# Kernel tuning notes

Hardware: AMD Instinct MI355X
Metric: run time of the kernel (lower is better)

Reference implementation:

```python
import jax, jax.numpy as jnp
import numpy as np
import math

H_IMG, W_IMG = 800, 1216
STRIDES = [4, 8, 16, 32, 64]
SIZES = [32, 64, 128, 256, 512]
RATIOS = [0.5, 1.0, 2.0]
NUM_PER_LEVEL = [(-(-H_IMG // s)) * (-(-W_IMG // s)) * len(RATIOS) for s in STRIDES]
A_TOTAL = sum(NUM_PER_LEVEL)  # 728973
B = 4
PRE_NMS = 1000   # pre_nms_top_n['testing']
POST_NMS = 1000  # post_nms_top_n['testing']
NMS_TH = 0.7
MIN_SIZE = 1e-3
BBOX_XFORM_CLIP = math.log(1000.0 / 16)
NEG = -1e10
LEVELS_NP = np.repeat(np.arange(len(NUM_PER_LEVEL)), NUM_PER_LEVEL).astype(np.int32)


def _make_anchors():
    out = []
    for stride, size in zip(STRIDES, SIZES):
        fh, fw = -(-H_IMG // stride), -(-W_IMG // stride)
        r = np.sqrt(np.asarray(RATIOS, dtype=np.float64))
        ws, hs = size / r, size * r
        base = np.stack([-ws / 2, -hs / 2, ws / 2, hs / 2], axis=1)  # [3,4]
        sx = np.arange(fw, dtype=np.float64) * stride
        sy = np.arange(fh, dtype=np.float64) * stride
        gy, gx = np.meshgrid(sy, sx, indexing='ij')
        shifts = np.stack([gx.ravel(), gy.ravel(), gx.ravel(), gy.ravel()], axis=1)
        out.append((shifts[:, None, :] + base[None]).reshape(-1, 4))
    return np.concatenate(out, 0).astype(np.float32)


def setup_inputs() -> dict:
    key = jax.random.key(0)
    k1, k2 = jax.random.split(key)
    objectness = jax.random.normal(k1, (B, A_TOTAL), dtype=jnp.float32)
    deltas = jax.random.normal(k2, (B, A_TOTAL, 4), dtype=jnp.float32) * 0.2
    anchors = jnp.asarray(_make_anchors())
    return {'objectness': objectness, 'deltas': deltas, 'anchors': anchors}


def _decode(deltas, anchors):
    # BoxCoder.decode with weights (1,1,1,1)
    wa = anchors[:, 2] - anchors[:, 0]
    ha = anchors[:, 3] - anchors[:, 1]
    cxa = anchors[:, 0] + 0.5 * wa
    cya = anchors[:, 1] + 0.5 * ha
    dx, dy = deltas[..., 0], deltas[..., 1]
    dw = jnp.minimum(deltas[..., 2], BBOX_XFORM_CLIP)
    dh = jnp.minimum(deltas[..., 3], BBOX_XFORM_CLIP)
    cx = dx * wa + cxa
    cy = dy * ha + cya
    w = jnp.exp(dw) * wa
    h = jnp.exp(dh) * ha
    return jnp.stack([cx - 0.5 * w, cy - 0.5 * h, cx + 0.5 * w, cy + 0.5 * h], axis=-1)


def _topk_per_level(obj):
    # _get_top_n_idx: independent top-k within each anchor level, indices offset
    idxs, off = [], 0
    for n in NUM_PER_LEVEL:
        k = min(PRE_NMS, n)
        _, ti = jax.lax.top_k(obj[:, off:off + n], k)
        idxs.append(ti + off)
        off += n
    return jnp.concatenate(idxs, axis=1)


def _pairwise_iou(b):
    area = (b[:, 2] - b[:, 0]) * (b[:, 3] - b[:, 1])
    lt = jnp.maximum(b[:, None, :2], b[None, :, :2])
    rb = jnp.minimum(b[:, None, 2:], b[None, :, 2:])
    wh = jnp.clip(rb - lt, 0.0)
    inter = wh[..., 0] * wh[..., 1]
    return inter / (area[:, None] + area[None, :] - inter)


def _filter_image(boxes, scores, lvl):
    # clip_boxes_to_image
    x1 = jnp.clip(boxes[:, 0], 0.0, W_IMG)
    y1 = jnp.clip(boxes[:, 1], 0.0, H_IMG)
    x2 = jnp.clip(boxes[:, 2], 0.0, W_IMG)
    y2 = jnp.clip(boxes[:, 3], 0.0, H_IMG)
    boxes = jnp.stack([x1, y1, x2, y2], axis=1)
    # remove_small_boxes (as a validity mask; fixed shapes under jit)
    valid = ((x2 - x1) >= MIN_SIZE) & ((y2 - y1) >= MIN_SIZE)
    scores = jnp.where(valid, scores, NEG)
    N = boxes.shape[0]
    # batched_nms: offset boxes per level so levels never overlap
    sg_boxes = jax.lax.stop_gradient(boxes)
    offset = lvl.astype(boxes.dtype) * (sg_boxes.max() + 1.0)
    order = jnp.argsort(-jax.lax.stop_gradient(scores))
    iou = _pairwise_iou(sg_boxes[order] + offset[order][:, None])  # [N,N]
    idx = jnp.arange(N)
    def body(i, keep):
        sup = (iou[i] > NMS_TH) & keep[i] & (idx > i)
        return keep & ~sup
    keep = jax.lax.fori_loop(0, N, body, valid[order])
    # kept entries in score order, then truncate to POST_NMS (fixed shape)
    prio = jnp.where(keep, idx, N)
    sel = jnp.argsort(prio)[:POST_NMS]
    kept = keep[sel]
    src = order[sel]
    out_b = jnp.where(kept[:, None], boxes[src], 0.0)
    out_s = jnp.where(kept, scores[src], NEG)
    return out_b, out_s


def reference(objectness, deltas, anchors):
    proposals = _decode(deltas, anchors)                      # [B,A,4]
    top_idx = _topk_per_level(objectness)                     # [B,5000]
    obj_sel = jnp.take_along_axis(objectness, top_idx, axis=1)
    prop_sel = jnp.take_along_axis(proposals, top_idx[..., None], axis=1)
    lvl_sel = jnp.asarray(LEVELS_NP)[top_idx]
    boxes, scores = jax.vmap(_filter_image)(prop_sel, obj_sel, lvl_sel)
    return boxes, scores  # [B,POST_NMS,4], [B,POST_NMS]
```

## Files before the change

### kernel.cpp

```cpp
#include <hip/hip_runtime.h>
#include <stdint.h>

#pragma clang fp contract(off)

#define B_IMGS   4
#define NLVL     5
#define A_TOTAL  242991
#define NSEL     4741
#define NBUCK    8192
#define BSHIFT   19
#define CAND_CAP 2048
#define POST_NMS 1000
#define NBL      (B_IMGS * NLVL)
#define NMS_TH   0.7f
#define NEGV     (-1e10f)
#define W_IMGF   1216.0f
#define H_IMGF   800.0f
#define MIN_SZ   1e-3f
#define BBOX_CLIP 4.135166556742356f

__device__ __forceinline__ int lvl_k(int l) { return (l == 4) ? 741 : 1000; }

__device__ __forceinline__ unsigned flipf(float f) {
    unsigned u = __float_as_uint(f);
    return u ^ (unsigned)(((int)u >> 31) | 0x80000000);
}
__device__ __forceinline__ float unflipf(unsigned os) {
    unsigned u = (os & 0x80000000u) ? (os ^ 0x80000000u) : ~os;
    return __uint_as_float(u);
}

__device__ __forceinline__ void async_cp16(const void* g, void* l) {
    __builtin_amdgcn_global_load_lds(
        (const __attribute__((address_space(1))) unsigned*)g,
        (__attribute__((address_space(3))) unsigned*)l,
        16, 0, 0);
}

static constexpr size_t SZ_HIST    = (size_t)NBL * NBUCK * sizeof(unsigned);
static constexpr size_t OFF_CNT    = SZ_HIST;
static constexpr size_t OFF_BOXMAX = OFF_CNT + NBL * sizeof(unsigned);
static constexpr size_t ZERO_BYTES = OFF_BOXMAX + B_IMGS * sizeof(unsigned);
static constexpr size_t OFF_CAND   = (ZERO_BYTES + 15) & ~(size_t)15;
static constexpr size_t OFF_SEL    = OFF_CAND + (size_t)NBL * CAND_CAP * 8;
static constexpr size_t OFF_BOXR   = OFF_SEL + (size_t)B_IMGS * NSEL * 8;
static constexpr size_t OFF_SCR    = OFF_BOXR + (size_t)B_IMGS * NSEL * 16;
static constexpr size_t OFF_BOXL   = OFF_SCR + (size_t)B_IMGS * NSEL * 4;
static constexpr size_t OFF_VAL    = OFF_BOXL + (size_t)B_IMGS * NSEL * 16;
static constexpr size_t OFF_RMAP   = OFF_VAL + (size_t)B_IMGS * NSEL * 4;
static constexpr size_t OFF_KEEP   = OFF_RMAP + (size_t)B_IMGS * NSEL * 4;
static constexpr size_t OFF_MASK   = OFF_KEEP + (size_t)B_IMGS * NSEL * 4;
static constexpr size_t WS_NEED    = OFF_MASK + (size_t)NBL * 1024 * 16 * 8;

#define HBLK_PER_IMG 34
__global__ void k_hist(const float* __restrict__ obj, unsigned* __restrict__ hist) {
    __shared__ unsigned lh[NBUCK];
    const int tid = threadIdx.x;
    const int b = blockIdx.x / HBLK_PER_IMG;
    const int r = blockIdx.x - b * HBLK_PER_IMG;
    int l, sub, chunk, lstart, n;
    if (r < 24)      { l = 0; sub = r;      chunk = 7600; lstart = 0;      n = 182400; }
    else if (r < 30) { l = 1; sub = r - 24; chunk = 7600; lstart = 182400; n = 45600; }
    else if (r < 32) { l = 2; sub = r - 30; chunk = 5700; lstart = 228000; n = 11400; }
    else if (r == 32){ l = 3; sub = 0;      chunk = 2850; lstart = 239400; n = 2850; }
    else             { l = 4; sub = 0;      chunk = 741;  lstart = 242250; n = 741; }
    #pragma unroll
    for (int i = tid; i < NBUCK; i += 512) lh[i] = 0;
    __syncthreads();
    const int s0 = sub * chunk;
    const int cnt = min(chunk, n - s0);
    const float* src = obj + (size_t)b * A_TOTAL + lstart + s0;
    for (int i = tid; i < cnt; i += 512) {
        unsigned os = flipf(src[i]);
        atomicAdd(&lh[os >> BSHIFT], 1u);
    }
    __syncthreads();
    unsigned* gh = hist + (size_t)(b * NLVL + l) * NBUCK;
    for (int i = tid; i < NBUCK; i += 512) {
        unsigned v = lh[i];
        if (v) atomicAdd(&gh[i], v);
    }
}

#define CBLK_PER_IMG 65
__global__ void k_compact(const float* __restrict__ obj, const unsigned* __restrict__ hist,
                          unsigned* __restrict__ cnt, unsigned long long* __restrict__ cand) {
    __shared__ unsigned long long sbuf[CAND_CAP];
    __shared__ unsigned part[256];
    __shared__ unsigned chunkbuf[32];
    __shared__ int s_chunk;
    __shared__ unsigned s_cum, s_thr, lcnt, gbase;
    const int tid = threadIdx.x;
    const int b = blockIdx.x / CBLK_PER_IMG;
    const int r = blockIdx.x - b * CBLK_PER_IMG;
    int l, sub, chunk, lstart, n;
    if (r < 48)      { l = 0; sub = r;      chunk = 3800; lstart = 0;      n = 182400; }
    else if (r < 60) { l = 1; sub = r - 48; chunk = 3800; lstart = 182400; n = 45600; }
    else if (r < 63) { l = 2; sub = r - 60; chunk = 3800; lstart = 228000; n = 11400; }
    else if (r == 63){ l = 3; sub = 0;      chunk = 2850; lstart = 239400; n = 2850; }
    else             { l = 4; sub = 0;      chunk = 741;  lstart = 242250; n = 741; }
    const int bl = b * NLVL + l;
    const int kl = lvl_k(l);
    const unsigned* h = hist + (size_t)bl * NBUCK;
    {
        unsigned s = 0;
        for (int i = 0; i < 32; ++i) s += h[tid * 32 + i];
        part[tid] = s;
    }
    if (tid == 0) lcnt = 0;
    __syncthreads();
    if (tid == 0) {
        unsigned cum = 0;
        int t = 255;
        for (; t > 0; --t) {
            if (cum + part[t] >= (unsigned)kl) break;
            cum += part[t];
        }
        s_chunk = t;
        s_cum = cum;
    }
    __syncthreads();
    if (tid < 32) chunkbuf[tid] = h[s_chunk * 32 + tid];
    __syncthreads();
    if (tid == 0) {
        unsigned c2 = s_cum;
        int T = s_chunk * 32;
        for (int i = 31; i >= 0; --i) {
            c2 += chunkbuf[i];
            if (c2 >= (unsigned)kl) { T = s_chunk * 32 + i; break; }
        }
        s_thr = (unsigned)T;
    }
    __syncthreads();
    const unsigned T = s_thr;
    const int s0 = sub * chunk;
    const int m = min(chunk, n - s0);
    const int abase = lstart + s0;
    const float* src = obj + (size_t)b * A_TOTAL + abase;
    for (int i = tid; i < m; i += 256) {
        unsigned os = flipf(src[i]);
        if ((os >> BSHIFT) >= T) {
            unsigned slot = atomicAdd(&lcnt, 1u);
            if (slot < CAND_CAP)
                sbuf[slot] = (((unsigned long long)(~os)) << 32) | (unsigned)(abase + i);
        }
    }
    __syncthreads();
    unsigned total = lcnt; if (total > CAND_CAP) total = CAND_CAP;
    if (tid == 0) gbase = atomicAdd(&cnt[bl], total);
    __syncthreads();
    const unsigned gb = gbase;
    for (unsigned i = tid; i < total; i += 256) {
        unsigned g = gb + i;
        if (g < CAND_CAP)
            cand[(size_t)bl * CAND_CAP + g] = sbuf[i];
    }
}

__global__ void k_sortlevel(const unsigned long long* __restrict__ cand,
                            const unsigned* __restrict__ cnt,
                            unsigned long long* __restrict__ sel) {
    __shared__ unsigned long long keys[CAND_CAP];
    const int bl = blockIdx.x;
    const int b = bl / NLVL, l = bl - (bl / NLVL) * NLVL;
    const int tid = threadIdx.x;
    int m = (int)cnt[bl];
    if (m > CAND_CAP) m = CAND_CAP;
    for (int i = tid; i < CAND_CAP; i += 512)
        keys[i] = (i < m) ? cand[(size_t)bl * CAND_CAP + i] : ~0ULL;
    __syncthreads();
    for (int k = 2; k <= CAND_CAP; k <<= 1) {
        for (int j = k >> 1; j > 0; j >>= 1) {
            for (int t = tid; t < CAND_CAP / 2; t += 512) {
                int i = ((t / j) * (j << 1)) + (t % j);
                int p = i + j;
                bool up = ((i & k) == 0);
                unsigned long long a = keys[i], c = keys[p];
                if ((a > c) == up) { keys[i] = c; keys[p] = a; }
            }
            __syncthreads();
        }
    }
    int kl = lvl_k(l);
    for (int q = tid; q < kl; q += 512)
        sel[(size_t)b * NSEL + l * 1000 + q] = keys[q];
}

__device__ __forceinline__ int lbound_lds(const unsigned long long* s, int len,
                                          unsigned long long key) {
    int lo = 0, hi = len;
    while (lo < hi) {
        int mid = (lo + hi) >> 1;
        if (s[mid] < key) lo = mid + 1; else hi = mid;
    }
    return lo;
}

__global__ void k_decode(const float* __restrict__ deltas, const float* __restrict__ anchors,
                         const unsigned long long* __restrict__ sel,
                         float* __restrict__ boxes_r, float* __restrict__ score_r,
                         float* __restrict__ boxes_l, int* __restrict__ valid_l,
                         int* __restrict__ rankmap, unsigned* __restrict__ boxmax) {
    __shared__ unsigned long long skey[NSEL];
    __shared__ float wmax[16];
    const int b = blockIdx.y;
    const int tid = threadIdx.x;
    for (int i = tid; i < NSEL; i += 1024)
        skey[i] = sel[(size_t)b * NSEL + i];
    __syncthreads();

    int p = blockIdx.x * 1024 + tid;
    bool on = p < NSEL;
    float mx = 0.0f;
    if (on) {
        int l = p / 1000;
        int q = p - l * 1000;
        unsigned long long key = skey[p];
        unsigned a = (unsigned)(key & 0xFFFFFFFFu);
        unsigned os = ~((unsigned)(key >> 32));
        if (a >= A_TOTAL) a = 0;
        float score = unflipf(os);
        int r = q;
        for (int l2 = 0; l2 < NLVL; ++l2) {
            if (l2 == l) continue;
            r += lbound_lds(skey + l2 * 1000, lvl_k(l2), key);
        }
        const float* dv = deltas + ((size_t)b * A_TOTAL + a) * 4;
        const float* av = anchors + (size_t)a * 4;
        float ax1 = av[0], ay1 = av[1], ax2 = av[2], ay2 = av[3];
        float wa = ax2 - ax1, ha = ay2 - ay1;
        float cxa = ax1 + 0.5f * wa, cya = ay1 + 0.5f * ha;
        float dx = dv[0], dy = dv[1];
        float dw = fminf(dv[2], BBOX_CLIP), dh = fminf(dv[3], BBOX_CLIP);
        float cx = dx * wa + cxa, cy = dy * ha + cya;
        float w = expf(dw) * wa, h = expf(dh) * ha;
        float x1 = cx - 0.5f * w, y1 = cy - 0.5f * h;
        float x2 = cx + 0.5f * w, y2 = cy + 0.5f * h;
        float x1c = fminf(fmaxf(x1, 0.0f), W_IMGF);
        float y1c = fminf(fmaxf(y1, 0.0f), H_IMGF);
        float x2c = fminf(fmaxf(x2, 0.0f), W_IMGF);
        float y2c = fminf(fmaxf(y2, 0.0f), H_IMGF);
        int valid = ((x2c - x1c) >= MIN_SZ) && ((y2c - y1c) >= MIN_SZ);
        mx = fmaxf(fmaxf(x1c, y1c), fmaxf(x2c, y2c));
        size_t rp = (size_t)b * NSEL + r;
        boxes_r[rp * 4 + 0] = x1c; boxes_r[rp * 4 + 1] = y1c;
        boxes_r[rp * 4 + 2] = x2c; boxes_r[rp * 4 + 3] = y2c;
        score_r[rp] = score;
        size_t pp = (size_t)b * NSEL + p;
        boxes_l[pp * 4 + 0] = x1c; boxes_l[pp * 4 + 1] = y1c;
        boxes_l[pp * 4 + 2] = x2c; boxes_l[pp * 4 + 3] = y2c;
        valid_l[pp] = valid;
        rankmap[pp] = r;
    }
    #pragma unroll
    for (int o = 32; o > 0; o >>= 1)
        mx = fmaxf(mx, __shfl_xor(mx, o));
    if ((tid & 63) == 0) wmax[tid >> 6] = mx;
    __syncthreads();
    if (tid == 0) {
        float m2 = wmax[0];
        #pragma unroll
        for (int i = 1; i < 16; ++i) m2 = fmaxf(m2, wmax[i]);
        atomicMax(boxmax + b, __float_as_uint(m2));
    }
}

__global__ void k_mask(const float* __restrict__ boxes_l, const unsigned* __restrict__ boxmax,
                       unsigned long long* __restrict__ mask) {
    int bl = blockIdx.z;
    int b = bl / NLVL, l = bl - b * NLVL;
    int kl = lvl_k(l);
    int w = blockIdx.x, rg = blockIdx.y, tid = threadIdx.x;
    if (rg * 256 >= kl) return;
    float M = __uint_as_float(boxmax[b]) + 1.0f;
    float off = (float)l * M;
    __shared__ float cb[64][5];
    int j0 = w * 64;
    if (tid < 64) {
        int j = j0 + tid;
        if (j < kl) {
            const float* bp = boxes_l + ((size_t)b * NSEL + l * 1000 + j) * 4;
            float x1 = bp[0] + off, y1 = bp[1] + off, x2 = bp[2] + off, y2 = bp[3] + off;
            cb[tid][0] = x1; cb[tid][1] = y1; cb[tid][2] = x2; cb[tid][3] = y2;
            cb[tid][4] = (x2 - x1) * (y2 - y1);
        }
    }
    __syncthreads();
    int i = rg * 256 + tid;
    if (i >= kl) return;
    unsigned long long word = 0;
    if (j0 + 63 > i) {
        const float* bp = boxes_l + ((size_t)b * NSEL + l * 1000 + i) * 4;
        float ix1 = bp[0] + off, iy1 = bp[1] + off, ix2 = bp[2] + off, iy2 = bp[3] + off;
        float ai = (ix2 - ix1) * (iy2 - iy1);
        int jmax = min(64, kl - j0);
        for (int bb = 0; bb < jmax; ++bb) {
            int jj = j0 + bb;
            if (jj <= i) continue;
            float ltx = fmaxf(ix1, cb[bb][0]), lty = fmaxf(iy1, cb[bb][1]);
            float rbx = fminf(ix2, cb[bb][2]), rby = fminf(iy2, cb[bb][3]);
            float ww = fmaxf(rbx - ltx, 0.0f), hh = fmaxf(rby - lty, 0.0f);
            float inter = ww * hh;
            float iou = inter / ((ai + cb[bb][4]) - inter);
            if (iou > NMS_TH) word |= (1ULL << bb);
        }
    }
    mask[((size_t)bl * 1024 + i) * 16 + w] = word;
}

__global__ void k_resolve(const int* __restrict__ valid_l, const int* __restrict__ rankmap,
                          const unsigned long long* __restrict__ mask, int* __restrict__ keep_r) {
    const int bl = blockIdx.x;
    const int b = bl / NLVL, l = bl - b * NLVL;
    const int kl = lvl_k(l);
    const int lane = threadIdx.x;
    __shared__ __align__(16) unsigned long long sbufA[64 * 16];
    __shared__ __align__(16) unsigned long long sbufB[64 * 16];
    const int base = b * NSEL + l * 1000;

    unsigned long long keep_w = 0;
    for (int c = 0; c < 16; ++c) {
        int q = c * 64 + lane;
        int vv = (q < kl) ? valid_l[base + q] : 0;
        unsigned long long bm = __ballot(vv);
        if (lane == c) keep_w = bm;
    }

    const int nch = (kl + 63) >> 6;
    const char* mbyte = (const char*)(mask + (size_t)bl * 1024 * 16);

    {
        const char* g0 = mbyte + (size_t)lane * 16;
        #pragma unroll
        for (int j = 0; j < 8; ++j)
            async_cp16(g0 + j * 1024, (char*)sbufA + j * 1024);
    }

    for (int c = 0; c < nch; ++c) {
        unsigned long long* cur = (c & 1) ? sbufB : sbufA;
        unsigned long long* nxt = (c & 1) ? sbufA : sbufB;
        __syncthreads();
        if (c + 1 < nch) {
            const char* g1 = mbyte + (size_t)(c + 1) * 8192 + (size_t)lane * 16;
            #pragma unroll
            for (int j = 0; j < 8; ++j)
                async_cp16(g1 + j * 1024, (char*)nxt + j * 1024);
        }
        unsigned long long kw = __shfl(keep_w, c);
        if (kw) {
            unsigned long long diag = cur[lane * 16 + c];
            unsigned dlo = (unsigned)diag, dhi = (unsigned)(diag >> 32);
            unsigned long long nz = __ballot(diag != 0ULL);
            unsigned long long rem = kw & nz;
            while (rem) {
                int r = __ffsll((long long)rem) - 1;
                unsigned lo = __builtin_amdgcn_readlane(dlo, r);
                unsigned hi = __builtin_amdgcn_readlane(dhi, r);
                unsigned long long d = ((unsigned long long)hi << 32) | lo;
                kw &= ~d;
                rem &= ~(d | (1ULL << r));
            }
            unsigned long long supp = 0;
            if (lane < 16) {
                #pragma unroll
                for (int r = 0; r < 64; ++r) {
                    unsigned long long m = cur[r * 16 + lane];
                    supp |= (((kw >> r) & 1ULL) ? m : 0ULL);
                }
            }
            if (lane == c) keep_w = kw;
            else if (lane < 16 && lane > c) keep_w &= ~supp;
        }
    }
    __syncthreads();
    for (int c = 0; c < 16; ++c) {
        unsigned long long kwc = __shfl(keep_w, c);
        int q = c * 64 + lane;
        if (q < kl)
            keep_r[b * NSEL + rankmap[base + q]] = (int)((kwc >> lane) & 1ULL);
    }
}

__global__ void k_output(const int* __restrict__ keep_r, const float* __restrict__ boxes_r,
                         const float* __restrict__ score_r, float* __restrict__ out) {
    int b = blockIdx.x, tid = threadIdx.x;
    float* ob = out + (size_t)b * POST_NMS * 4;
    float* osc = out + (size_t)B_IMGS * POST_NMS * 4 + (size_t)b * POST_NMS;
    for (int p = tid; p < POST_NMS; p += 1024) {
        ob[p * 4 + 0] = 0.0f; ob[p * 4 + 1] = 0.0f;
        ob[p * 4 + 2] = 0.0f; ob[p * 4 + 3] = 0.0f;
        osc[p] = NEGV;
    }
    __syncthreads();
    const int CH = 5;
    int base = tid * CH;
    int cnt = 0;
    #pragma unroll
    for (int k = 0; k < CH; ++k) {
        int r = base + k;
        if (r < NSEL) cnt += keep_r[b * NSEL + r];
    }
    __shared__ int ps[1024];
    ps[tid] = cnt;
    __syncthreads();
    for (int ofs = 1; ofs < 1024; ofs <<= 1) {
        int v = (tid >= ofs) ? ps[tid - ofs] : 0;
        __syncthreads();
        ps[tid] += v;
        __syncthreads();
    }
    int p = ps[tid] - cnt;
    #pragma unroll
    for (int k = 0; k < CH; ++k) {
        int r = base + k;
        if (r < NSEL && keep_r[b * NSEL + r]) {
            if (p < POST_NMS) {
                const float* bp = boxes_r + ((size_t)b * NSEL + r) * 4;
                ob[p * 4 + 0] = bp[0]; ob[p * 4 + 1] = bp[1];
                ob[p * 4 + 2] = bp[2]; ob[p * 4 + 3] = bp[3];
                osc[p] = score_r[(size_t)b * NSEL + r];
            }
            ++p;
        }
    }
}

extern "C" void kernel_launch(void* const* d_in, const int* in_sizes, int n_in,
                              void* d_out, int out_size, void* d_ws, size_t ws_size,
                              hipStream_t stream) {
    const float* obj     = (const float*)d_in[0];
    const float* deltas  = (const float*)d_in[1];
    const float* anchors = (const float*)d_in[2];
    float* out = (float*)d_out;

    char* ws = (char*)d_ws;
    unsigned*            hist    = (unsigned*)(ws);
    unsigned*            cnt     = (unsigned*)(ws + OFF_CNT);
    unsigned*            boxmax  = (unsigned*)(ws + OFF_BOXMAX);
    unsigned long long*  cand    = (unsigned long long*)(ws + OFF_CAND);
    unsigned long long*  sel     = (unsigned long long*)(ws + OFF_SEL);
    float*               boxes_r = (float*)(ws + OFF_BOXR);
    float*               score_r = (float*)(ws + OFF_SCR);
    float*               boxes_l = (float*)(ws + OFF_BOXL);
    int*                 valid_l = (int*)(ws + OFF_VAL);
    int*                 rankmap = (int*)(ws + OFF_RMAP);
    int*                 keep_r  = (int*)(ws + OFF_KEEP);
    unsigned long long*  maskp   = (unsigned long long*)(ws + OFF_MASK);

    (void)in_sizes; (void)n_in; (void)out_size; (void)ws_size; (void)WS_NEED;

    hipMemsetAsync(d_ws, 0, ZERO_BYTES, stream);

    k_hist<<<B_IMGS * HBLK_PER_IMG, 512, 0, stream>>>(obj, hist);
    k_compact<<<B_IMGS * CBLK_PER_IMG, 256, 0, stream>>>(obj, hist, cnt, cand);
    k_sortlevel<<<NBL, 512, 0, stream>>>(cand, cnt, sel);
    k_decode<<<dim3(5, B_IMGS), 1024, 0, stream>>>(
        deltas, anchors, sel, boxes_r, score_r, boxes_l, valid_l, rankmap, boxmax);
    k_mask<<<dim3(16, 4, NBL), 256, 0, stream>>>(boxes_l, boxmax, maskp);
    k_resolve<<<NBL, 64, 0, stream>>>(valid_l, rankmap, maskp, keep_r);
    k_output<<<B_IMGS, 1024, 0, stream>>>(keep_r, boxes_r, score_r, out);
}
```

Baseline: 193.5 us.

## Fuse all RPN stages into one persistent kernel with grid barriers

Replaces seven separate kernel launches with a single persistent kernel of 136 blocks that runs histogram, compaction, per-level sort, decode, mask building, NMS resolve and output as phases separated by atomic-counter grid barriers. This removes per-launch overhead and the idle gaps between small dependent kernels. The price is less parallelism in some phases (compaction uses 136 blocks instead of 260, mask work is looped over blocks), fixed block sizes for every stage, and correctness that depends on all blocks being co-resident.

New measurement: 246.9 us. 1.28x slower.

```diff
diff --git a/kernel.cpp b/kernel.cpp
--- a/kernel.cpp
+++ b/kernel.cpp
@@ -19,7 +19,20 @@
 #define MIN_SZ   1e-3f
 #define BBOX_CLIP 4.135166556742356f
 
+#define NBLK     136
+#define BLKT     512
+#define HBLK_PER_IMG 34
+
 __device__ __forceinline__ int lvl_k(int l) { return (l == 4) ? 741 : 1000; }
+
+__device__ __forceinline__ void span34(int r, int& l, int& sub, int& chunk,
+                                       int& lstart, int& n) {
+    if (r < 24)      { l = 0; sub = r;      chunk = 7600; lstart = 0;      n = 182400; }
+    else if (r < 30) { l = 1; sub = r - 24; chunk = 7600; lstart = 182400; n = 45600; }
+    else if (r < 32) { l = 2; sub = r - 30; chunk = 5700; lstart = 228000; n = 11400; }
+    else if (r == 32){ l = 3; sub = 0;      chunk = 2850; lstart = 239400; n = 2850; }
+    else             { l = 4; sub = 0;      chunk = 741;  lstart = 242250; n = 741; }
+}
 
 __device__ __forceinline__ unsigned flipf(float f) {
     unsigned u = __float_as_uint(f);
@@ -37,10 +50,33 @@
         16, 0, 0);
 }
 
+__device__ __forceinline__ int lbound_lds(const unsigned long long* s, int len,
+                                          unsigned long long key) {
+    int lo = 0, hi = len;
+    while (lo < hi) {
+        int mid = (lo + hi) >> 1;
+        if (s[mid] < key) lo = mid + 1; else hi = mid;
+    }
+    return lo;
+}
+
+__device__ __forceinline__ void gbar(unsigned* bar, unsigned target) {
+    __syncthreads();
+    if (threadIdx.x == 0) {
+        __threadfence();
+        __hip_atomic_fetch_add(bar, 1u, __ATOMIC_RELAXED, __HIP_MEMORY_SCOPE_AGENT);
+        while (__hip_atomic_load(bar, __ATOMIC_RELAXED, __HIP_MEMORY_SCOPE_AGENT) < target)
+            __builtin_amdgcn_s_sleep(8);
+        __threadfence();
+    }
+    __syncthreads();
+}
+
 static constexpr size_t SZ_HIST    = (size_t)NBL * NBUCK * sizeof(unsigned);
 static constexpr size_t OFF_CNT    = SZ_HIST;
 static constexpr size_t OFF_BOXMAX = OFF_CNT + NBL * sizeof(unsigned);
-static constexpr size_t ZERO_BYTES = OFF_BOXMAX + B_IMGS * sizeof(unsigned);
+static constexpr size_t OFF_BAR    = OFF_BOXMAX + B_IMGS * sizeof(unsigned);
+static constexpr size_t ZERO_BYTES = OFF_BAR + 16;
 static constexpr size_t OFF_CAND   = (ZERO_BYTES + 15) & ~(size_t)15;
 static constexpr size_t OFF_SEL    = OFF_CAND + (size_t)NBL * CAND_CAP * 8;
 static constexpr size_t OFF_BOXR   = OFF_SEL + (size_t)B_IMGS * NSEL * 8;
@@ -52,375 +88,372 @@
 static constexpr size_t OFF_MASK   = OFF_KEEP + (size_t)B_IMGS * NSEL * 4;
 static constexpr size_t WS_NEED    = OFF_MASK + (size_t)NBL * 1024 * 16 * 8;
 
-#define HBLK_PER_IMG 34
-__global__ void k_hist(const float* __restrict__ obj, unsigned* __restrict__ hist) {
-    __shared__ unsigned lh[NBUCK];
+__global__ __launch_bounds__(BLKT, 2) void k_fused(
+    const float* __restrict__ obj, const float* __restrict__ deltas,
+    const float* __restrict__ anchors,
+    unsigned* __restrict__ hist, unsigned* __restrict__ cnt,
+    unsigned* __restrict__ boxmax, unsigned* __restrict__ bar,
+    unsigned long long* __restrict__ cand, unsigned long long* __restrict__ sel,
+    float* __restrict__ boxes_r, float* __restrict__ score_r,
+    float* __restrict__ boxes_l, int* __restrict__ valid_l,
+    int* __restrict__ rankmap, int* __restrict__ keep_r,
+    unsigned long long* __restrict__ maskp, float* __restrict__ out)
+{
+    __shared__ __align__(16) char smem[38912];
     const int tid = threadIdx.x;
-    const int b = blockIdx.x / HBLK_PER_IMG;
-    const int r = blockIdx.x - b * HBLK_PER_IMG;
-    int l, sub, chunk, lstart, n;
-    if (r < 24)      { l = 0; sub = r;      chunk = 7600; lstart = 0;      n = 182400; }
-    else if (r < 30) { l = 1; sub = r - 24; chunk = 7600; lstart = 182400; n = 45600; }
-    else if (r < 32) { l = 2; sub = r - 30; chunk = 5700; lstart = 228000; n = 11400; }
-    else if (r == 32){ l = 3; sub = 0;      chunk = 2850; lstart = 239400; n = 2850; }
-    else             { l = 4; sub = 0;      chunk = 741;  lstart = 242250; n = 741; }
-    #pragma unroll
-    for (int i = tid; i < NBUCK; i += 512) lh[i] = 0;
-    __syncthreads();
-    const int s0 = sub * chunk;
-    const int cnt = min(chunk, n - s0);
-    const float* src = obj + (size_t)b * A_TOTAL + lstart + s0;
-    for (int i = tid; i < cnt; i += 512) {
-        unsigned os = flipf(src[i]);
-        atomicAdd(&lh[os >> BSHIFT], 1u);
-    }
-    __syncthreads();
-    unsigned* gh = hist + (size_t)(b * NLVL + l) * NBUCK;
-    for (int i = tid; i < NBUCK; i += 512) {
-        unsigned v = lh[i];
-        if (v) atomicAdd(&gh[i], v);
-    }
-}
-
-#define CBLK_PER_IMG 65
-__global__ void k_compact(const float* __restrict__ obj, const unsigned* __restrict__ hist,
-                          unsigned* __restrict__ cnt, unsigned long long* __restrict__ cand) {
-    __shared__ unsigned long long sbuf[CAND_CAP];
-    __shared__ unsigned part[256];
-    __shared__ unsigned chunkbuf[32];
-    __shared__ int s_chunk;
-    __shared__ unsigned s_cum, s_thr, lcnt, gbase;
-    const int tid = threadIdx.x;
-    const int b = blockIdx.x / CBLK_PER_IMG;
-    const int r = blockIdx.x - b * CBLK_PER_IMG;
-    int l, sub, chunk, lstart, n;
-    if (r < 48)      { l = 0; sub = r;      chunk = 3800; lstart = 0;      n = 182400; }
-    else if (r < 60) { l = 1; sub = r - 48; chunk = 3800; lstart = 182400; n = 45600; }
-    else if (r < 63) { l = 2; sub = r - 60; chunk = 3800; lstart = 228000; n = 11400; }
-    else if (r == 63){ l = 3; sub = 0;      chunk = 2850; lstart = 239400; n = 2850; }
-    else             { l = 4; sub = 0;      chunk = 741;  lstart = 242250; n = 741; }
-    const int bl = b * NLVL + l;
-    const int kl = lvl_k(l);
-    const unsigned* h = hist + (size_t)bl * NBUCK;
+    const int bid = blockIdx.x;
+
     {
-        unsigned s = 0;
-        for (int i = 0; i < 32; ++i) s += h[tid * 32 + i];
-        part[tid] = s;
-    }
-    if (tid == 0) lcnt = 0;
-    __syncthreads();
-    if (tid == 0) {
-        unsigned cum = 0;
-        int t = 255;
-        for (; t > 0; --t) {
-            if (cum + part[t] >= (unsigned)kl) break;
-            cum += part[t];
-        }
-        s_chunk = t;
-        s_cum = cum;
-    }
-    __syncthreads();
-    if (tid < 32) chunkbuf[tid] = h[s_chunk * 32 + tid];
-    __syncthreads();
-    if (tid == 0) {
-        unsigned c2 = s_cum;
-        int T = s_chunk * 32;
-        for (int i = 31; i >= 0; --i) {
-            c2 += chunkbuf[i];
-            if (c2 >= (unsigned)kl) { T = s_chunk * 32 + i; break; }
-        }
-        s_thr = (unsigned)T;
-    }
-    __syncthreads();
-    const unsigned T = s_thr;
-    const int s0 = sub * chunk;
-    const int m = min(chunk, n - s0);
-    const int abase = lstart + s0;
-    const float* src = obj + (size_t)b * A_TOTAL + abase;
-    for (int i = tid; i < m; i += 256) {
-        unsigned os = flipf(src[i]);
-        if ((os >> BSHIFT) >= T) {
-            unsigned slot = atomicAdd(&lcnt, 1u);
-            if (slot < CAND_CAP)
-                sbuf[slot] = (((unsigned long long)(~os)) << 32) | (unsigned)(abase + i);
-        }
-    }
-    __syncthreads();
-    unsigned total = lcnt; if (total > CAND_CAP) total = CAND_CAP;
-    if (tid == 0) gbase = atomicAdd(&cnt[bl], total);
-    __syncthreads();
-    const unsigned gb = gbase;
-    for (unsigned i = tid; i < total; i += 256) {
-        unsigned g = gb + i;
-        if (g < CAND_CAP)
-            cand[(size_t)bl * CAND_CAP + g] = sbuf[i];
-    }
-}
-
-__global__ void k_sortlevel(const unsigned long long* __restrict__ cand,
-                            const unsigned* __restrict__ cnt,
-                            unsigned long long* __restrict__ sel) {
-    __shared__ unsigned long long keys[CAND_CAP];
-    const int bl = blockIdx.x;
-    const int b = bl / NLVL, l = bl - (bl / NLVL) * NLVL;
-    const int tid = threadIdx.x;
-    int m = (int)cnt[bl];
-    if (m > CAND_CAP) m = CAND_CAP;
-    for (int i = tid; i < CAND_CAP; i += 512)
-        keys[i] = (i < m) ? cand[(size_t)bl * CAND_CAP + i] : ~0ULL;
-    __syncthreads();
-    for (int k = 2; k <= CAND_CAP; k <<= 1) {
-        for (int j = k >> 1; j > 0; j >>= 1) {
-            for (int t = tid; t < CAND_CAP / 2; t += 512) {
-                int i = ((t / j) * (j << 1)) + (t % j);
-                int p = i + j;
-                bool up = ((i & k) == 0);
-                unsigned long long a = keys[i], c = keys[p];
-                if ((a > c) == up) { keys[i] = c; keys[p] = a; }
-            }
+        unsigned* lh = (unsigned*)smem;
+        const int b = bid / HBLK_PER_IMG;
+        const int r = bid - b * HBLK_PER_IMG;
+        int l, sub, chunk, lstart, n;
+        span34(r, l, sub, chunk, lstart, n);
+        for (int i = tid; i < NBUCK; i += BLKT) lh[i] = 0;
+        __syncthreads();
+        const int s0 = sub * chunk;
+        const int m = min(chunk, n - s0);
+        const float* src = obj + (size_t)b * A_TOTAL + lstart + s0;
+        for (int i = tid; i < m; i += BLKT) {
+            unsigned os = flipf(src[i]);
+            atomicAdd(&lh[os >> BSHIFT], 1u);
+        }
+        __syncthreads();
+        unsigned* gh = hist + (size_t)(b * NLVL + l) * NBUCK;
+        for (int i = tid; i < NBUCK; i += BLKT) {
+            unsigned v = lh[i];
+            if (v) atomicAdd(&gh[i], v);
+        }
+    }
+    gbar(bar, 1u * NBLK);
+
+    {
+        unsigned long long* sbuf = (unsigned long long*)smem;
+        unsigned* part     = (unsigned*)(smem + 16384);
+        unsigned* chunkbuf = (unsigned*)(smem + 17408);
+        int*      s_chunk  = (int*)     (smem + 17536);
+        unsigned* s_cum    = (unsigned*)(smem + 17540);
+        unsigned* s_thr    = (unsigned*)(smem + 17544);
+        unsigned* lcnt     = (unsigned*)(smem + 17548);
+        unsigned* gbase    = (unsigned*)(smem + 17552);
+        const int b = bid / HBLK_PER_IMG;
+        const int r = bid - b * HBLK_PER_IMG;
+        int l, sub, chunk, lstart, n;
+        span34(r, l, sub, chunk, lstart, n);
+        const int bl = b * NLVL + l;
+        const int kl = lvl_k(l);
+        const unsigned* h = hist + (size_t)bl * NBUCK;
+        if (tid < 256) {
+            unsigned s = 0;
+            for (int i = 0; i < 32; ++i) s += h[tid * 32 + i];
+            part[tid] = s;
+        }
+        if (tid == 0) *lcnt = 0;
+        __syncthreads();
+        if (tid == 0) {
+            unsigned cum = 0;
+            int t = 255;
+            for (; t > 0; --t) {
+                if (cum + part[t] >= (unsigned)kl) break;
+                cum += part[t];
+            }
+            *s_chunk = t;
+            *s_cum = cum;
+        }
+        __syncthreads();
+        if (tid < 32) chunkbuf[tid] = h[(*s_chunk) * 32 + tid];
+        __syncthreads();
+        if (tid == 0) {
+            unsigned c2 = *s_cum;
+            int T = (*s_chunk) * 32;
+            for (int i = 31; i >= 0; --i) {
+                c2 += chunkbuf[i];
+                if (c2 >= (unsigned)kl) { T = (*s_chunk) * 32 + i; break; }
+            }
+            *s_thr = (unsigned)T;
+        }
+        __syncthreads();
+        const unsigned T = *s_thr;
+        const int s0 = sub * chunk;
+        const int m = min(chunk, n - s0);
+        const int abase = lstart + s0;
+        const float* src = obj + (size_t)b * A_TOTAL + abase;
+        for (int i = tid; i < m; i += BLKT) {
+            unsigned os = flipf(src[i]);
+            if ((os >> BSHIFT) >= T) {
+                unsigned slot = atomicAdd(lcnt, 1u);
+                if (slot < CAND_CAP)
+                    sbuf[slot] = (((unsigned long long)(~os)) << 32) | (unsigned)(abase + i);
+            }
+        }
+        __syncthreads();
+        unsigned total = *lcnt; if (total > CAND_CAP) total = CAND_CAP;
+        if (tid == 0) *gbase = atomicAdd(&cnt[bl], total);
+        __syncthreads();
+        const unsigned gb = *gbase;
+        for (unsigned i = tid; i < total; i += BLKT) {
+            unsigned g = gb + i;
+            if (g < CAND_CAP)
+                cand[(size_t)bl * CAND_CAP + g] = sbuf[i];
+        }
+    }
+    gbar(bar, 2u * NBLK);
+
+    if (bid < NBL) {
+        unsigned long long* keys = (unsigned long long*)smem;
+        const int bl = bid;
+        const int b = bl / NLVL, l = bl - b * NLVL;
+        int m = (int)cnt[bl];
+        if (m > CAND_CAP) m = CAND_CAP;
+        for (int i = tid; i < CAND_CAP; i += BLKT)
+            keys[i] = (i < m) ? cand[(size_t)bl * CAND_CAP + i] : ~0ULL;
+        __syncthreads();
+        for (int k = 2; k <= CAND_CAP; k <<= 1) {
+            for (int j = k >> 1; j > 0; j >>= 1) {
+                for (int t = tid; t < CAND_CAP / 2; t += BLKT) {
+                    int i = ((t / j) * (j << 1)) + (t % j);
+                    int p = i + j;
+                    bool up = ((i & k) == 0);
+                    unsigned long long a = keys[i], c = keys[p];
+                    if ((a > c) == up) { keys[i] = c; keys[p] = a; }
+                }
+                __syncthreads();
+            }
+        }
+        int kl = lvl_k(l);
+        for (int q = tid; q < kl; q += BLKT)
+            sel[(size_t)b * NSEL + l * 1000 + q] = keys[q];
+    }
+    gbar(bar, 3u * NBLK);
+
+    if (bid < B_IMGS * 10) {
+        unsigned long long* skey = (unsigned long long*)smem;
+        float* wmax = (float*)(smem + 37928);
+        const int b = bid / 10;
+        const int sub = bid - b * 10;
+        for (int i = tid; i < NSEL; i += BLKT)
+            skey[i] = sel[(size_t)b * NSEL + i];
+        __syncthreads();
+
+        int p = sub * BLKT + tid;
+        bool on = p < NSEL;
+        float mx = 0.0f;
+        if (on) {
+            int l = p / 1000;
+            int q = p - l * 1000;
+            unsigned long long key = skey[p];
+            unsigned a = (unsigned)(key & 0xFFFFFFFFu);
+            unsigned os = ~((unsigned)(key >> 32));
+            if (a >= A_TOTAL) a = 0;
+            float score = unflipf(os);
+            int r = q;
+            for (int l2 = 0; l2 < NLVL; ++l2) {
+                if (l2 == l) continue;
+                r += lbound_lds(skey + l2 * 1000, lvl_k(l2), key);
+            }
+            const float* dv = deltas + ((size_t)b * A_TOTAL + a) * 4;
+            const float* av = anchors + (size_t)a * 4;
+            float ax1 = av[0], ay1 = av[1], ax2 = av[2], ay2 = av[3];
+            float wa = ax2 - ax1, ha = ay2 - ay1;
+            float cxa = ax1 + 0.5f * wa, cya = ay1 + 0.5f * ha;
+            float dx = dv[0], dy = dv[1];
+            float dw = fminf(dv[2], BBOX_CLIP), dh = fminf(dv[3], BBOX_CLIP);
+            float cx = dx * wa + cxa, cy = dy * ha + cya;
+            float w = expf(dw) * wa, h = expf(dh) * ha;
+            float x1 = cx - 0.5f * w, y1 = cy - 0.5f * h;
+            float x2 = cx + 0.5f * w, y2 = cy + 0.5f * h;
+            float x1c = fminf(fmaxf(x1, 0.0f), W_IMGF);
+            float y1c = fminf(fmaxf(y1, 0.0f), H_IMGF);
+            float x2c = fminf(fmaxf(x2, 0.0f), W_IMGF);
+            float y2c = fminf(fmaxf(y2, 0.0f), H_IMGF);
+            int valid = ((x2c - x1c) >= MIN_SZ) && ((y2c - y1c) >= MIN_SZ);
+            mx = fmaxf(fmaxf(x1c, y1c), fmaxf(x2c, y2c));
+            size_t rp = (size_t)b * NSEL + r;
+            boxes_r[rp * 4 + 0] = x1c; boxes_r[rp * 4 + 1] = y1c;
+            boxes_r[rp * 4 + 2] = x2c; boxes_r[rp * 4 + 3] = y2c;
+            score_r[rp] = score;
+            size_t pp = (size_t)b * NSEL + p;
+            boxes_l[pp * 4 + 0] = x1c; boxes_l[pp * 4 + 1] = y1c;
+            boxes_l[pp * 4 + 2] = x2c; boxes_l[pp * 4 + 3] = y2c;
+            valid_l[pp] = valid;
+            rankmap[pp] = r;
+        }
+        #pragma unroll
+        for (int o = 32; o > 0; o >>= 1)
+            mx = fmaxf(mx, __shfl_xor(mx, o));
+        if ((tid & 63) == 0) wmax[tid >> 6] = mx;
+        __syncthreads();
+        if (tid == 0) {
+            float m2 = wmax[0];
+            #pragma unroll
+            for (int i = 1; i < 8; ++i) m2 = fmaxf(m2, wmax[i]);
+            atomicMax(boxmax + b, __float_as_uint(m2));
+        }
+    }
+    gbar(bar, 4u * NBLK);
+
+    {
+        float (*cb)[5] = (float(*)[5])smem;
+        for (int u = bid; u < 640; u += NBLK) {
+            int w = u & 15, rg2 = (u >> 4) & 1, bl = u >> 5;
+            int b = bl / NLVL, l = bl - b * NLVL;
+            int kl = lvl_k(l);
+            bool act = (rg2 * BLKT < kl);
+            float M = __uint_as_float(boxmax[b]) + 1.0f;
+            float off = (float)l * M;
+            int j0 = w * 64;
             __syncthreads();
-        }
-    }
-    int kl = lvl_k(l);
-    for (int q = tid; q < kl; q += 512)
-        sel[(size_t)b * NSEL + l * 1000 + q] = keys[q];
-}
-
-__device__ __forceinline__ int lbound_lds(const unsigned long long* s, int len,
-                                          unsigned long long key) {
-    int lo = 0, hi = len;
-    while (lo < hi) {
-        int mid = (lo + hi) >> 1;
-        if (s[mid] < key) lo = mid + 1; else hi = mid;
-    }
-    return lo;
-}
-
-__global__ void k_decode(const float* __restrict__ deltas, const float* __restrict__ anchors,
-                         const unsigned long long* __restrict__ sel,
-                         float* __restrict__ boxes_r, float* __restrict__ score_r,
-                         float* __restrict__ boxes_l, int* __restrict__ valid_l,
-                         int* __restrict__ rankmap, unsigned* __restrict__ boxmax) {
-    __shared__ unsigned long long skey[NSEL];
-    __shared__ float wmax[16];
-    const int b = blockIdx.y;
-    const int tid = threadIdx.x;
-    for (int i = tid; i < NSEL; i += 1024)
-        skey[i] = sel[(size_t)b * NSEL + i];
-    __syncthreads();
-
-    int p = blockIdx.x * 1024 + tid;
-    bool on = p < NSEL;
-    float mx = 0.0f;
-    if (on) {
-        int l = p / 1000;
-        int q = p - l * 1000;
-        unsigned long long key = skey[p];
-        unsigned a = (unsigned)(key & 0xFFFFFFFFu);
-        unsigned os = ~((unsigned)(key >> 32));
-        if (a >= A_TOTAL) a = 0;
-        float score = unflipf(os);
-        int r = q;
-        for (int l2 = 0; l2 < NLVL; ++l2) {
-            if (l2 == l) continue;
-            r += lbound_lds(skey + l2 * 1000, lvl_k(l2), key);
-        }
-        const float* dv = deltas + ((size_t)b * A_TOTAL + a) * 4;
-        const float* av = anchors + (size_t)a * 4;
-        float ax1 = av[0], ay1 = av[1], ax2 = av[2], ay2 = av[3];
-        float wa = ax2 - ax1, ha = ay2 - ay1;
-        float cxa = ax1 + 0.5f * wa, cya = ay1 + 0.5f * ha;
-        float dx = dv[0], dy = dv[1];
-        float dw = fminf(dv[2], BBOX_CLIP), dh = fminf(dv[3], BBOX_CLIP);
-        float cx = dx * wa + cxa, cy = dy * ha + cya;
-        float w = expf(dw) * wa, h = expf(dh) * ha;
-        float x1 = cx - 0.5f * w, y1 = cy - 0.5f * h;
-        float x2 = cx + 0.5f * w, y2 = cy + 0.5f * h;
-        float x1c = fminf(fmaxf(x1, 0.0f), W_IMGF);
-        float y1c = fminf(fmaxf(y1, 0.0f), H_IMGF);
-        float x2c = fminf(fmaxf(x2, 0.0f), W_IMGF);
-        float y2c = fminf(fmaxf(y2, 0.0f), H_IMGF);
-        int valid = ((x2c - x1c) >= MIN_SZ) && ((y2c - y1c) >= MIN_SZ);
-        mx = fmaxf(fmaxf(x1c, y1c), fmaxf(x2c, y2c));
-        size_t rp = (size_t)b * NSEL + r;
-        boxes_r[rp * 4 + 0] = x1c; boxes_r[rp * 4 + 1] = y1c;
-        boxes_r[rp * 4 + 2] = x2c; boxes_r[rp * 4 + 3] = y2c;
-        score_r[rp] = score;
-        size_t pp = (size_t)b * NSEL + p;
-        boxes_l[pp * 4 + 0] = x1c; boxes_l[pp * 4 + 1] = y1c;
-        boxes_l[pp * 4 + 2] = x2c; boxes_l[pp * 4 + 3] = y2c;
-        valid_l[pp] = valid;
-        rankmap[pp] = r;
-    }
-    #pragma unroll
-    for (int o = 32; o > 0; o >>= 1)
-        mx = fmaxf(mx, __shfl_xor(mx, o));
-    if ((tid & 63) == 0) wmax[tid >> 6] = mx;
-    __syncthreads();
-    if (tid == 0) {
-        float m2 = wmax[0];
-        #pragma unroll
-        for (int i = 1; i < 16; ++i) m2 = fmaxf(m2, wmax[i]);
-        atomicMax(boxmax + b, __float_as_uint(m2));
-    }
-}
-
-__global__ void k_mask(const float* __restrict__ boxes_l, const unsigned* __restrict__ boxmax,
-                       unsigned long long* __restrict__ mask) {
-    int bl = blockIdx.z;
-    int b = bl / NLVL, l = bl - b * NLVL;
-    int kl = lvl_k(l);
-    int w = blockIdx.x, rg = blockIdx.y, tid = threadIdx.x;
-    if (rg * 256 >= kl) return;
-    float M = __uint_as_float(boxmax[b]) + 1.0f;
-    float off = (float)l * M;
-    __shared__ float cb[64][5];
-    int j0 = w * 64;
-    if (tid < 64) {
-        int j = j0 + tid;
-        if (j < kl) {
-            const float* bp = boxes_l + ((size_t)b * NSEL + l * 1000 + j) * 4;
-            float x1 = bp[0] + off, y1 = bp[1] + off, x2 = bp[2] + off, y2 = bp[3] + off;
-            cb[tid][0] = x1; cb[tid][1] = y1; cb[tid][2] = x2; cb[tid][3] = y2;
-            cb[tid][4] = (x2 - x1) * (y2 - y1);
-        }
-    }
-    __syncthreads();
-    int i = rg * 256 + tid;
-    if (i >= kl) return;
-    unsigned long long word = 0;
-    if (j0 + 63 > i) {
-        const float* bp = boxes_l + ((size_t)b * NSEL + l * 1000 + i) * 4;
-        float ix1 = bp[0] + off, iy1 = bp[1] + off, ix2 = bp[2] + off, iy2 = bp[3] + off;
-        float ai = (ix2 - ix1) * (iy2 - iy1);
-        int jmax = min(64, kl - j0);
-        for (int bb = 0; bb < jmax; ++bb) {
-            int jj = j0 + bb;
-            if (jj <= i) continue;
-            float ltx = fmaxf(ix1, cb[bb][0]), lty = fmaxf(iy1, cb[bb][1]);
-            float rbx = fminf(ix2, cb[bb][2]), rby = fminf(iy2, cb[bb][3]);
-            float ww = fmaxf(rbx - ltx, 0.0f), hh = fmaxf(rby - lty, 0.0f);
-            float inter = ww * hh;
-            float iou = inter / ((ai + cb[bb][4]) - inter);
-            if (iou > NMS_TH) word |= (1ULL << bb);
-        }
-    }
-    mask[((size_t)bl * 1024 + i) * 16 + w] = word;
-}
-
-__global__ void k_resolve(const int* __restrict__ valid_l, const int* __restrict__ rankmap,
-                          const unsigned long long* __restrict__ mask, int* __restrict__ keep_r) {
-    const int bl = blockIdx.x;
-    const int b = bl / NLVL, l = bl - b * NLVL;
-    const int kl = lvl_k(l);
-    const int lane = threadIdx.x;
-    __shared__ __align__(16) unsigned long long sbufA[64 * 16];
-    __shared__ __align__(16) unsigned long long sbufB[64 * 16];
-    const int base = b * NSEL + l * 1000;
-
-    unsigned long long keep_w = 0;
-    for (int c = 0; c < 16; ++c) {
-        int q = c * 64 + lane;
-        int vv = (q < kl) ? valid_l[base + q] : 0;
-        unsigned long long bm = __ballot(vv);
-        if (lane == c) keep_w = bm;
-    }
-
-    const int nch = (kl + 63) >> 6;
-    const char* mbyte = (const char*)(mask + (size_t)bl * 1024 * 16);
-
-    {
-        const char* g0 = mbyte + (size_t)lane * 16;
-        #pragma unroll
-        for (int j = 0; j < 8; ++j)
-            async_cp16(g0 + j * 1024, (char*)sbufA + j * 1024);
-    }
-
-    for (int c = 0; c < nch; ++c) {
-        unsigned long long* cur = (c & 1) ? sbufB : sbufA;
-        unsigned long long* nxt = (c & 1) ? sbufA : sbufB;
-        __syncthreads();
-        if (c + 1 < nch) {
-            const char* g1 = mbyte + (size_t)(c + 1) * 8192 + (size_t)lane * 16;
+            if (act && tid < 64) {
+                int j = j0 + tid;
+                if (j < kl) {
+                    const float* bp = boxes_l + ((size_t)b * NSEL + l * 1000 + j) * 4;
+                    float x1 = bp[0] + off, y1 = bp[1] + off;
+                    float x2 = bp[2] + off, y2 = bp[3] + off;
+                    cb[tid][0] = x1; cb[tid][1] = y1; cb[tid][2] = x2; cb[tid][3] = y2;
+                    cb[tid][4] = (x2 - x1) * (y2 - y1);
+                }
+            }
+            __syncthreads();
+            int i = rg2 * BLKT + tid;
+            if (act && i < kl) {
+                unsigned long long word = 0;
+                if (j0 + 63 > i) {
+                    const float* bp = boxes_l + ((size_t)b * NSEL + l * 1000 + i) * 4;
+                    float ix1 = bp[0] + off, iy1 = bp[1] + off;
+                    float ix2 = bp[2] + off, iy2 = bp[3] + off;
+                    float ai = (ix2 - ix1) * (iy2 - iy1);
+                    int jmax = min(64, kl - j0);
+                    for (int bb = 0; bb < jmax; ++bb) {
+                        int jj = j0 + bb;
+                        if (jj <= i) continue;
+                        float ltx = fmaxf(ix1, cb[bb][0]), lty = fmaxf(iy1, cb[bb][1]);
+                        float rbx = fminf(ix2, cb[bb][2]), rby = fminf(iy2, cb[bb][3]);
+                        float ww = fmaxf(rbx - ltx, 0.0f), hh = fmaxf(rby - lty, 0.0f);
+                        float inter = ww * hh;
+                        float iou = inter / ((ai + cb[bb][4]) - inter);
+                        if (iou > NMS_TH) word |= (1ULL << bb);
+                    }
+                }
+                maskp[((size_t)bl * 1024 + i) * 16 + w] = word;
+            }
+        }
+    }
+    gbar(bar, 5u * NBLK);
+
+    if (bid < NBL) {
+        const int bl = bid;
+        const int b = bl / NLVL, l = bl - b * NLVL;
+        const int kl = lvl_k(l);
+        const int lane = tid;
+        unsigned long long* sA = (unsigned long long*)smem;
+        unsigned long long* sB = (unsigned long long*)(smem + 8192);
+        const int base = b * NSEL + l * 1000;
+        unsigned long long keep_w = 0;
+        const int nch = (kl + 63) >> 6;
+        const char* mbyte = (const char*)(maskp + (size_t)bl * 1024 * 16);
+
+        if (tid < 64) {
+            for (int c = 0; c < 16; ++c) {
+                int q = c * 64 + lane;
+                int vv = (q < kl) ? valid_l[base + q] : 0;
+                unsigned long long bm = __ballot(vv);
+                if (lane == c) keep_w = bm;
+            }
+            const char* g0 = mbyte + (size_t)lane * 16;
             #pragma unroll
             for (int j = 0; j < 8; ++j)
-                async_cp16(g1 + j * 1024, (char*)nxt + j * 1024);
-        }
-        unsigned long long kw = __shfl(keep_w, c);
-        if (kw) {
-            unsigned long long diag = cur[lane * 16 + c];
-            unsigned dlo = (unsigned)diag, dhi = (unsigned)(diag >> 32);
-            unsigned long long nz = __ballot(diag != 0ULL);
-            unsigned long long rem = kw & nz;
-            while (rem) {
-                int r = __ffsll((long long)rem) - 1;
-                unsigned lo = __builtin_amdgcn_readlane(dlo, r);
-                unsigned hi = __builtin_amdgcn_readlane(dhi, r);
-                unsigned long long d = ((unsigned long long)hi << 32) | lo;
-                kw &= ~d;
-                rem &= ~(d | (1ULL << r));
-            }
-            unsigned long long supp = 0;
-            if (lane < 16) {
-                #pragma unroll
-                for (int r = 0; r < 64; ++r) {
-                    unsigned long long m = cur[r * 16 + lane];
-                    supp |= (((kw >> r) & 1ULL) ? m : 0ULL);
-                }
-            }
-            if (lane == c) keep_w = kw;
-            else if (lane < 16 && lane > c) keep_w &= ~supp;
-        }
-    }
-    __syncthreads();
-    for (int c = 0; c < 16; ++c) {
-        unsigned long long kwc = __shfl(keep_w, c);
-        int q = c * 64 + lane;
-        if (q < kl)
-            keep_r[b * NSEL + rankmap[base + q]] = (int)((kwc >> lane) & 1ULL);
-    }
-}
-
-__global__ void k_output(const int* __restrict__ keep_r, const float* __restrict__ boxes_r,
-                         const float* __restrict__ score_r, float* __restrict__ out) {
-    int b = blockIdx.x, tid = threadIdx.x;
-    float* ob = out + (size_t)b * POST_NMS * 4;
-    float* osc = out + (size_t)B_IMGS * POST_NMS * 4 + (size_t)b * POST_NMS;
-    for (int p = tid; p < POST_NMS; p += 1024) {
-        ob[p * 4 + 0] = 0.0f; ob[p * 4 + 1] = 0.0f;
-        ob[p * 4 + 2] = 0.0f; ob[p * 4 + 3] = 0.0f;
-        osc[p] = NEGV;
-    }
-    __syncthreads();
-    const int CH = 5;
-    int base = tid * CH;
-    int cnt = 0;
-    #pragma unroll
-    for (int k = 0; k < CH; ++k) {
-        int r = base + k;
-        if (r < NSEL) cnt += keep_r[b * NSEL + r];
-    }
-    __shared__ int ps[1024];
-    ps[tid] = cnt;
-    __syncthreads();
-    for (int ofs = 1; ofs < 1024; ofs <<= 1) {
-        int v = (tid >= ofs) ? ps[tid - ofs] : 0;
-        __syncthreads();
-        ps[tid] += v;
-        __syncthreads();
-    }
-    int p = ps[tid] - cnt;
-    #pragma unroll
-    for (int k = 0; k < CH; ++k) {
-        int r = base + k;
-        if (r < NSEL && keep_r[b * NSEL + r]) {
-            if (p < POST_NMS) {
-                const float* bp = boxes_r + ((size_t)b * NSEL + r) * 4;
-                ob[p * 4 + 0] = bp[0]; ob[p * 4 + 1] = bp[1];
-                ob[p * 4 + 2] = bp[2]; ob[p * 4 + 3] = bp[3];
-                osc[p] = score_r[(size_t)b * NSEL + r];
-            }
-            ++p;
+                async_cp16(g0 + j * 1024, (char*)sA + j * 1024);
+        }
+        for (int c = 0; c < nch; ++c) {
+            __syncthreads();
+            if (tid < 64) {
+                unsigned long long* cur = (c & 1) ? sB : sA;
+                unsigned long long* nxt = (c & 1) ? sA : sB;
+                if (c + 1 < nch) {
+                    const char* g1 = mbyte + (size_t)(c + 1) * 8192 + (size_t)lane * 16;
+                    #pragma unroll
+                    for (int j = 0; j < 8; ++j)
+                        async_cp16(g1 + j * 1024, (char*)nxt + j * 1024);
+                }
+                unsigned long long kw = __shfl(keep_w, c);
+                if (kw) {
+                    unsigned long long diag = cur[lane * 16 + c];
+                    unsigned dlo = (unsigned)diag, dhi = (unsigned)(diag >> 32);
+                    unsigned long long nz = __ballot(diag != 0ULL);
+                    unsigned long long rem = kw & nz;
+                    while (rem) {
+                        int rr = __ffsll((long long)rem) - 1;
+                        unsigned lo = __builtin_amdgcn_readlane(dlo, rr);
+                        unsigned hi = __builtin_amdgcn_readlane(dhi, rr);
+                        unsigned long long d = ((unsigned long long)hi << 32) | lo;
+                        kw &= ~d;
+                        rem &= ~(d | (1ULL << rr));
+                    }
+                    unsigned long long supp = 0;
+                    if (lane < 16) {
+                        #pragma unroll
+                        for (int rr = 0; rr < 64; ++rr) {
+                            unsigned long long mm = cur[rr * 16 + lane];
+                            supp |= (((kw >> rr) & 1ULL) ? mm : 0ULL);
+                        }
+                    }
+                    if (lane == c) keep_w = kw;
+                    else if (lane < 16 && lane > c) keep_w &= ~supp;
+                }
+            }
+        }
+        __syncthreads();
+        if (tid < 64) {
+            for (int c = 0; c < 16; ++c) {
+                unsigned long long kwc = __shfl(keep_w, c);
+                int q = c * 64 + lane;
+                if (q < kl)
+                    keep_r[b * NSEL + rankmap[base + q]] = (int)((kwc >> lane) & 1ULL);
+            }
+        }
+    }
+    gbar(bar, 6u * NBLK);
+
+    if (bid < B_IMGS) {
+        int* ps = (int*)smem;
+        const int b = bid;
+        float* ob = out + (size_t)b * POST_NMS * 4;
+        float* osc = out + (size_t)B_IMGS * POST_NMS * 4 + (size_t)b * POST_NMS;
+        for (int p = tid; p < POST_NMS; p += BLKT) {
+            ob[p * 4 + 0] = 0.0f; ob[p * 4 + 1] = 0.0f;
+            ob[p * 4 + 2] = 0.0f; ob[p * 4 + 3] = 0.0f;
+            osc[p] = NEGV;
+        }
+        __syncthreads();
+        const int CH = 10;
+        int basei = tid * CH;
+        int c0 = 0;
+        #pragma unroll
+        for (int k = 0; k < CH; ++k) {
+            int rr = basei + k;
+            if (rr < NSEL) c0 += keep_r[b * NSEL + rr];
+        }
+        ps[tid] = c0;
+        __syncthreads();
+        for (int ofs = 1; ofs < BLKT; ofs <<= 1) {
+            int v = (tid >= ofs) ? ps[tid - ofs] : 0;
+            __syncthreads();
+            ps[tid] += v;
+            __syncthreads();
+        }
+        int p = ps[tid] - c0;
+        #pragma unroll
+        for (int k = 0; k < CH; ++k) {
+            int rr = basei + k;
+            if (rr < NSEL && keep_r[b * NSEL + rr]) {
+                if (p < POST_NMS) {
+                    const float* bp = boxes_r + ((size_t)b * NSEL + rr) * 4;
+                    ob[p * 4 + 0] = bp[0]; ob[p * 4 + 1] = bp[1];
+                    ob[p * 4 + 2] = bp[2]; ob[p * 4 + 3] = bp[3];
+                    osc[p] = score_r[(size_t)b * NSEL + rr];
+                }
+                ++p;
+            }
         }
     }
 }
@@ -437,6 +470,7 @@
     unsigned*            hist    = (unsigned*)(ws);
     unsigned*            cnt     = (unsigned*)(ws + OFF_CNT);
     unsigned*            boxmax  = (unsigned*)(ws + OFF_BOXMAX);
+    unsigned*            bar     = (unsigned*)(ws + OFF_BAR);
     unsigned long long*  cand    = (unsigned long long*)(ws + OFF_CAND);
     unsigned long long*  sel     = (unsigned long long*)(ws + OFF_SEL);
     float*               boxes_r = (float*)(ws + OFF_BOXR);
@@ -451,12 +485,7 @@
 
     hipMemsetAsync(d_ws, 0, ZERO_BYTES, stream);
 
-    k_hist<<<B_IMGS * HBLK_PER_IMG, 512, 0, stream>>>(obj, hist);
-    k_compact<<<B_IMGS * CBLK_PER_IMG, 256, 0, stream>>>(obj, hist, cnt, cand);
-    k_sortlevel<<<NBL, 512, 0, stream>>>(cand, cnt, sel);
-    k_decode<<<dim3(5, B_IMGS), 1024, 0, stream>>>(
-        deltas, anchors, sel, boxes_r, score_r, boxes_l, valid_l, rankmap, boxmax);
-    k_mask<<<dim3(16, 4, NBL), 256, 0, stream>>>(boxes_l, boxmax, maskp);
-    k_resolve<<<NBL, 64, 0, stream>>>(valid_l, rankmap, maskp, keep_r);
-    k_output<<<B_IMGS, 1024, 0, stream>>>(keep_r, boxes_r, score_r, out);
-}
+    k_fused<<<NBLK, BLKT, 0, stream>>>(
+        obj, deltas, anchors, hist, cnt, boxmax, bar, cand, sel,
+        boxes_r, score_r, boxes_l, valid_l, rankmap, keep_r, maskp, out);
+}
```
